# Performance work log

Measured on AMD Instinct MI355X. Metric: run time of the kernel, lower is better.

The kernel has to match this reference:

```python
import jax, jax.numpy as jnp
import numpy as np

EPS = 1e-3  # Keras BatchNormalization default epsilon


def _bn(x, gamma, beta, mean, var):
    # inference batch norm, channels-last
    inv = gamma * jax.lax.rsqrt(var + EPS)
    return x * inv + (beta - mean * inv)


def setup_inputs() -> dict:
    key = jax.random.key(0)
    ks = jax.random.split(key, 13)
    B, D, H, W, C, F = 2, 48, 48, 48, 64, 128
    return {
        "x": jax.random.normal(ks[0], (B, D, H, W, C), dtype=jnp.float32),
        "dw_kernel": jax.random.normal(ks[1], (3, 3, 3, 1, C), dtype=jnp.float32) * 0.1,
        "dw_bias": jax.random.normal(ks[2], (C,), dtype=jnp.float32) * 0.1,
        "bn1_gamma": jax.random.uniform(ks[3], (C,), dtype=jnp.float32, minval=0.5, maxval=1.5),
        "bn1_beta": jax.random.normal(ks[4], (C,), dtype=jnp.float32) * 0.1,
        "bn1_mean": jax.random.normal(ks[5], (C,), dtype=jnp.float32) * 0.1,
        "bn1_var": jax.random.uniform(ks[6], (C,), dtype=jnp.float32, minval=0.5, maxval=1.5),
        "pw_kernel": jax.random.normal(ks[7], (C, F), dtype=jnp.float32) * 0.1,
        "pw_bias": jax.random.normal(ks[8], (F,), dtype=jnp.float32) * 0.1,
        "bn2_gamma": jax.random.uniform(ks[9], (F,), dtype=jnp.float32, minval=0.5, maxval=1.5),
        "bn2_beta": jax.random.normal(ks[10], (F,), dtype=jnp.float32) * 0.1,
        "bn2_mean": jax.random.normal(ks[11], (F,), dtype=jnp.float32) * 0.1,
        "bn2_var": jax.random.uniform(ks[12], (F,), dtype=jnp.float32, minval=0.5, maxval=1.5),
    }


def reference(x, dw_kernel, dw_bias, bn1_gamma, bn1_beta, bn1_mean, bn1_var,
              pw_kernel, pw_bias, bn2_gamma, bn2_beta, bn2_mean, bn2_var):
    C = x.shape[-1]
    # True depthwise conv3d (replaces the per-channel Python loop of Conv3D(1,...))
    y = jax.lax.conv_general_dilated(
        x, dw_kernel,
        window_strides=(1, 1, 1), padding="SAME",
        dimension_numbers=("NDHWC", "DHWIO", "NDHWC"),
        feature_group_count=C,
    ) + dw_bias
    y = jax.nn.relu(_bn(y, bn1_gamma, bn1_beta, bn1_mean, bn1_var))
    # pointwise 1x1x1 conv == channel GEMM
    z = jnp.einsum("bdhwc,cf->bdhwf", y, pw_kernel) + pw_bias
    z = jax.nn.relu(_bn(z, bn2_gamma, bn2_beta, bn2_mean, bn2_var))
    return z
```

## Files before the change

### kernel.cpp

```cpp
#include <hip/hip_runtime.h>
#include <hip/hip_bf16.h>

#define EPS 1e-3f

typedef __attribute__((ext_vector_type(8))) short short8;
typedef __attribute__((ext_vector_type(4))) float v4f;

__device__ __forceinline__ unsigned short f2bf(float f) {
    unsigned int u = __float_as_uint(f);
    unsigned int r = (u + 0x7fffu + ((u >> 16) & 1u)) >> 16;
    return (unsigned short)r;
}

__global__ __launch_bounds__(256) void prep_kernel(
    const float* __restrict__ dwb,
    const float* __restrict__ g1, const float* __restrict__ b1,
    const float* __restrict__ m1, const float* __restrict__ v1,
    const float* __restrict__ pw, const float* __restrict__ pwb,
    const float* __restrict__ g2, const float* __restrict__ b2,
    const float* __restrict__ m2, const float* __restrict__ v2,
    float* __restrict__ scale1, float* __restrict__ shift1,
    float* __restrict__ s2, float* __restrict__ t2,
    unsigned short* __restrict__ Wt)
{
    int tid = threadIdx.x;
    if (blockIdx.x == 0) {
        if (tid < 64) {
            float inv = g1[tid] * rsqrtf(v1[tid] + EPS);
            scale1[tid] = inv;
            shift1[tid] = dwb[tid] * inv + b1[tid] - m1[tid] * inv;
        }
        if (tid < 128) {
            float inv = g2[tid] * rsqrtf(v2[tid] + EPS);
            s2[tid] = inv;
            t2[tid] = pwb[tid] * inv + b2[tid] - m2[tid] * inv;
        }
    }
    int idx = blockIdx.x * 256 + tid;
    int j     = idx & 7;
    int lane  = (idx >> 3) & 63;
    int kstep = (idx >> 9) & 1;
    int ntile = idx >> 10;
    int k = kstep * 32 + (lane >> 4) * 8 + j;
    int f = ntile * 16 + (lane & 15);
    Wt[idx] = f2bf(pw[k * 128 + f]);
}

__global__ __launch_bounds__(256) void fused_kernel(
    const float* __restrict__ x,
    const float* __restrict__ wgt,
    const float* __restrict__ scale1,
    const float* __restrict__ shift1,
    const unsigned short* __restrict__ Wt,
    const float* __restrict__ s2,
    const float* __restrict__ t2,
    float* __restrict__ out)
{
    __shared__ float wS[27 * 64];
    __shared__ float sS[64];
    __shared__ float tS[64];
    __shared__ unsigned short yS[64 * 72];

    int tid = threadIdx.x;
    for (int i = tid; i < 27 * 64; i += 256) wS[i] = wgt[i];
    if (tid < 64) { sS[tid] = scale1[tid]; tS[tid] = shift1[tid]; }
    __syncthreads();

    int w0 = blockIdx.x * 16;
    int h0 = blockIdx.y * 4;
    int bd = blockIdx.z;
    int b  = bd / 48;
    int d  = bd % 48;

    int tx = tid & 15;
    int ty = tid >> 4;
    int c0 = tx * 4;
    int wq = ty & 3;
    int rh = ty >> 2;
    int w0t = w0 + wq * 4;
    int h   = h0 + rh;

    float4 acc[4];
    #pragma unroll
    for (int r = 0; r < 4; ++r) acc[r] = make_float4(0.f, 0.f, 0.f, 0.f);

    float mw[6];
    int   wcl[6];
    #pragma unroll
    for (int p = 0; p < 6; ++p) {
        int zw = w0t - 1 + p;
        mw[p]  = (zw >= 0 && zw < 48) ? 1.f : 0.f;
        wcl[p] = min(max(zw, 0), 47) * 64;
    }
    float mh[3];
    int   hcl[3];
    #pragma unroll
    for (int hh = 0; hh < 3; ++hh) {
        int zh = h + hh - 1;
        mh[hh]  = (zh >= 0 && zh < 48) ? 1.f : 0.f;
        hcl[hh] = min(max(zh, 0), 47) * 48 * 64;
    }

    #pragma unroll
    for (int dd = 0; dd < 3; ++dd) {
        int zd = d + dd - 1;
        float md = (zd >= 0 && zd < 48) ? 1.f : 0.f;
        int zdc = min(max(zd, 0), 47);
        const float* dp = x + (((long)b * 48 + zdc) * 48 * 48) * 64 + c0;

        float4 xv[3][6];
        #pragma unroll
        for (int hh = 0; hh < 3; ++hh) {
            const float* rowp = dp + hcl[hh];
            #pragma unroll
            for (int p = 0; p < 6; ++p)
                xv[hh][p] = *(const float4*)(rowp + wcl[p]);
        }
        #pragma unroll
        for (int hh = 0; hh < 3; ++hh) {
            float mdh = md * mh[hh];
            #pragma unroll
            for (int p = 0; p < 6; ++p) {
                float m = mdh * mw[p];
                xv[hh][p].x *= m; xv[hh][p].y *= m;
                xv[hh][p].z *= m; xv[hh][p].w *= m;
            }
        }
        #pragma unroll
        for (int hh = 0; hh < 3; ++hh) {
            #pragma unroll
            for (int ww = 0; ww < 3; ++ww) {
                const float4 wv = *(const float4*)(&wS[((dd * 3 + hh) * 3 + ww) * 64 + c0]);
                #pragma unroll
                for (int r = 0; r < 4; ++r) {
                    acc[r].x += xv[hh][r + ww].x * wv.x;
                    acc[r].y += xv[hh][r + ww].y * wv.y;
                    acc[r].z += xv[hh][r + ww].z * wv.z;
                    acc[r].w += xv[hh][r + ww].w * wv.w;
                }
            }
        }
    }

    {
        float4 s = *(const float4*)(&sS[c0]);
        float4 t = *(const float4*)(&tS[c0]);
        #pragma unroll
        for (int r = 0; r < 4; ++r) {
            ushort4 o;
            o.x = f2bf(fmaxf(acc[r].x * s.x + t.x, 0.f));
            o.y = f2bf(fmaxf(acc[r].y * s.y + t.y, 0.f));
            o.z = f2bf(fmaxf(acc[r].z * s.z + t.z, 0.f));
            o.w = f2bf(fmaxf(acc[r].w * s.w + t.w, 0.f));
            *(ushort4*)(&yS[(ty * 4 + r) * 72 + c0]) = o;
        }
    }
    __syncthreads();

    int wv   = tid >> 6;
    int lane = tid & 63;
    int lrow = lane & 15;
    int quad = lane >> 4;

    const short8 a0 = *(const short8*)(&yS[(wv * 16 + lrow) * 72 + quad * 8]);
    const short8 a1 = *(const short8*)(&yS[(wv * 16 + lrow) * 72 + 32 + quad * 8]);

    v4f g[8];
    #pragma unroll
    for (int n = 0; n < 8; ++n) g[n] = (v4f){0.f, 0.f, 0.f, 0.f};

    #pragma unroll
    for (int n = 0; n < 8; ++n) {
        short8 b0 = *(const short8*)(Wt + ((n * 2 + 0) * 64 + lane) * 8);
        short8 b1 = *(const short8*)(Wt + ((n * 2 + 1) * 64 + lane) * 8);
        g[n] = __builtin_amdgcn_mfma_f32_16x16x32_bf16(a0, b0, g[n], 0, 0, 0);
        g[n] = __builtin_amdgcn_mfma_f32_16x16x32_bf16(a1, b1, g[n], 0, 0, 0);
    }

    long base_out = ((((long)b * 48 + d) * 48 + (h0 + wv)) * 48 + w0) * 128;
    #pragma unroll
    for (int n = 0; n < 8; ++n) {
        int f = n * 16 + lrow;
        float sf = s2[f];
        float tf = t2[f];
        #pragma unroll
        for (int r = 0; r < 4; ++r) {
            float v = fmaxf(g[n][r] * sf + tf, 0.f);
            __builtin_nontemporal_store(v, &out[base_out + (quad * 4 + r) * 128 + f]);
        }
    }
}

extern "C" void kernel_launch(void* const* d_in, const int* in_sizes, int n_in,
                              void* d_out, int out_size, void* d_ws, size_t ws_size,
                              hipStream_t stream)
{
    const float* x   = (const float*)d_in[0];
    const float* dwk = (const float*)d_in[1];
    const float* dwb = (const float*)d_in[2];
    const float* g1  = (const float*)d_in[3];
    const float* b1  = (const float*)d_in[4];
    const float* m1  = (const float*)d_in[5];
    const float* v1  = (const float*)d_in[6];
    const float* pw  = (const float*)d_in[7];
    const float* pwb = (const float*)d_in[8];
    const float* g2  = (const float*)d_in[9];
    const float* b2  = (const float*)d_in[10];
    const float* m2  = (const float*)d_in[11];
    const float* v2  = (const float*)d_in[12];

    float* outp = (float*)d_out;

    float* scale1 = (float*)d_ws;
    float* shift1 = scale1 + 64;
    float* s2     = scale1 + 128;
    float* t2     = scale1 + 256;
    unsigned short* Wt = (unsigned short*)((char*)d_ws + 2048);

    hipLaunchKernelGGL(prep_kernel, dim3(32), dim3(256), 0, stream,
                       dwb, g1, b1, m1, v1, pw, pwb, g2, b2, m2, v2,
                       scale1, shift1, s2, t2, Wt);

    hipLaunchKernelGGL(fused_kernel, dim3(3, 12, 96), dim3(256), 0, stream,
                       x, dwk, scale1, shift1, Wt, s2, t2, outp);
}
```

Measured before the change: 216.9 us.

## Remap blocks to XCDs for L2 locality, branch on boundary masks, plain stores

Flattens the grid to 1D and remaps block IDs so that each of the 8 XCDs handles a contiguous range of 12 depth slices, so neighbouring depth slices that share halo input stay in the same L2. Replaces the per-element multiplicative boundary masks with branches on depth/height validity and masks only the edge W columns, skipping FMAs for out-of-range rows. Switches the output stores from nontemporal to regular stores. These trade more branch divergence at the edges, and possible cache pollution from the output, for less redundant input traffic and arithmetic.

```diff
diff --git a/kernel.cpp b/kernel.cpp
--- a/kernel.cpp
+++ b/kernel.cpp
@@ -66,11 +66,15 @@
     if (tid < 64) { sS[tid] = scale1[tid]; tS[tid] = shift1[tid]; }
     __syncthreads();
 
-    int w0 = blockIdx.x * 16;
-    int h0 = blockIdx.y * 4;
-    int bd = blockIdx.z;
-    int b  = bd / 48;
-    int d  = bd % 48;
+    int n   = blockIdx.x;
+    int xcd = n & 7;
+    int j   = n >> 3;
+    int bd  = xcd * 12 + (j % 12);
+    int s   = j / 12;
+    int w0  = (s % 3) * 16;
+    int h0  = (s / 3) * 4;
+    int b   = bd / 48;
+    int d   = bd % 48;
 
     int tx = tid & 15;
     int ty = tid >> 4;
@@ -84,27 +88,26 @@
     #pragma unroll
     for (int r = 0; r < 4; ++r) acc[r] = make_float4(0.f, 0.f, 0.f, 0.f);
 
-    float mw[6];
-    int   wcl[6];
-    #pragma unroll
-    for (int p = 0; p < 6; ++p) {
-        int zw = w0t - 1 + p;
-        mw[p]  = (zw >= 0 && zw < 48) ? 1.f : 0.f;
-        wcl[p] = min(max(zw, 0), 47) * 64;
-    }
-    float mh[3];
-    int   hcl[3];
+    float mwL = (w0t >= 1)  ? 1.f : 0.f;
+    float mwR = (w0t <= 43) ? 1.f : 0.f;
+    int wcl[6];
+    #pragma unroll
+    for (int p = 0; p < 6; ++p)
+        wcl[p] = min(max(w0t - 1 + p, 0), 47) * 64;
+
+    bool hok[3];
+    int  hcl[3];
     #pragma unroll
     for (int hh = 0; hh < 3; ++hh) {
         int zh = h + hh - 1;
-        mh[hh]  = (zh >= 0 && zh < 48) ? 1.f : 0.f;
+        hok[hh] = (zh >= 0 && zh < 48);
         hcl[hh] = min(max(zh, 0), 47) * 48 * 64;
     }
 
     #pragma unroll
     for (int dd = 0; dd < 3; ++dd) {
         int zd = d + dd - 1;
-        float md = (zd >= 0 && zd < 48) ? 1.f : 0.f;
+        bool dok = (zd >= 0 && zd < 48);
         int zdc = min(max(zd, 0), 47);
         const float* dp = x + (((long)b * 48 + zdc) * 48 * 48) * 64 + c0;
 
@@ -116,42 +119,41 @@
             for (int p = 0; p < 6; ++p)
                 xv[hh][p] = *(const float4*)(rowp + wcl[p]);
         }
-        #pragma unroll
-        for (int hh = 0; hh < 3; ++hh) {
-            float mdh = md * mh[hh];
+
+        if (dok) {
             #pragma unroll
-            for (int p = 0; p < 6; ++p) {
-                float m = mdh * mw[p];
-                xv[hh][p].x *= m; xv[hh][p].y *= m;
-                xv[hh][p].z *= m; xv[hh][p].w *= m;
-            }
-        }
-        #pragma unroll
-        for (int hh = 0; hh < 3; ++hh) {
-            #pragma unroll
-            for (int ww = 0; ww < 3; ++ww) {
-                const float4 wv = *(const float4*)(&wS[((dd * 3 + hh) * 3 + ww) * 64 + c0]);
-                #pragma unroll
-                for (int r = 0; r < 4; ++r) {
-                    acc[r].x += xv[hh][r + ww].x * wv.x;
-                    acc[r].y += xv[hh][r + ww].y * wv.y;
-                    acc[r].z += xv[hh][r + ww].z * wv.z;
-                    acc[r].w += xv[hh][r + ww].w * wv.w;
+            for (int hh = 0; hh < 3; ++hh) {
+                if (hok[hh]) {
+                    xv[hh][0].x *= mwL; xv[hh][0].y *= mwL;
+                    xv[hh][0].z *= mwL; xv[hh][0].w *= mwL;
+                    xv[hh][5].x *= mwR; xv[hh][5].y *= mwR;
+                    xv[hh][5].z *= mwR; xv[hh][5].w *= mwR;
+                    #pragma unroll
+                    for (int ww = 0; ww < 3; ++ww) {
+                        const float4 wv = *(const float4*)(&wS[((dd * 3 + hh) * 3 + ww) * 64 + c0]);
+                        #pragma unroll
+                        for (int r = 0; r < 4; ++r) {
+                            acc[r].x += xv[hh][r + ww].x * wv.x;
+                            acc[r].y += xv[hh][r + ww].y * wv.y;
+                            acc[r].z += xv[hh][r + ww].z * wv.z;
+                            acc[r].w += xv[hh][r + ww].w * wv.w;
+                        }
+                    }
                 }
             }
         }
     }
 
     {
-        float4 s = *(const float4*)(&sS[c0]);
-        float4 t = *(const float4*)(&tS[c0]);
+        float4 s1 = *(const float4*)(&sS[c0]);
+        float4 t1 = *(const float4*)(&tS[c0]);
         #pragma unroll
         for (int r = 0; r < 4; ++r) {
             ushort4 o;
-            o.x = f2bf(fmaxf(acc[r].x * s.x + t.x, 0.f));
-            o.y = f2bf(fmaxf(acc[r].y * s.y + t.y, 0.f));
-            o.z = f2bf(fmaxf(acc[r].z * s.z + t.z, 0.f));
-            o.w = f2bf(fmaxf(acc[r].w * s.w + t.w, 0.f));
+            o.x = f2bf(fmaxf(acc[r].x * s1.x + t1.x, 0.f));
+            o.y = f2bf(fmaxf(acc[r].y * s1.y + t1.y, 0.f));
+            o.z = f2bf(fmaxf(acc[r].z * s1.z + t1.z, 0.f));
+            o.w = f2bf(fmaxf(acc[r].w * s1.w + t1.w, 0.f));
             *(ushort4*)(&yS[(ty * 4 + r) * 72 + c0]) = o;
         }
     }
@@ -167,26 +169,26 @@
 
     v4f g[8];
     #pragma unroll
-    for (int n = 0; n < 8; ++n) g[n] = (v4f){0.f, 0.f, 0.f, 0.f};
-
-    #pragma unroll
-    for (int n = 0; n < 8; ++n) {
-        short8 b0 = *(const short8*)(Wt + ((n * 2 + 0) * 64 + lane) * 8);
-        short8 b1 = *(const short8*)(Wt + ((n * 2 + 1) * 64 + lane) * 8);
-        g[n] = __builtin_amdgcn_mfma_f32_16x16x32_bf16(a0, b0, g[n], 0, 0, 0);
-        g[n] = __builtin_amdgcn_mfma_f32_16x16x32_bf16(a1, b1, g[n], 0, 0, 0);
+    for (int nn = 0; nn < 8; ++nn) g[nn] = (v4f){0.f, 0.f, 0.f, 0.f};
+
+    #pragma unroll
+    for (int nn = 0; nn < 8; ++nn) {
+        short8 b0 = *(const short8*)(Wt + ((nn * 2 + 0) * 64 + lane) * 8);
+        short8 b1 = *(const short8*)(Wt + ((nn * 2 + 1) * 64 + lane) * 8);
+        g[nn] = __builtin_amdgcn_mfma_f32_16x16x32_bf16(a0, b0, g[nn], 0, 0, 0);
+        g[nn] = __builtin_amdgcn_mfma_f32_16x16x32_bf16(a1, b1, g[nn], 0, 0, 0);
     }
 
     long base_out = ((((long)b * 48 + d) * 48 + (h0 + wv)) * 48 + w0) * 128;
     #pragma unroll
-    for (int n = 0; n < 8; ++n) {
-        int f = n * 16 + lrow;
+    for (int nn = 0; nn < 8; ++nn) {
+        int f = nn * 16 + lrow;
         float sf = s2[f];
         float tf = t2[f];
         #pragma unroll
         for (int r = 0; r < 4; ++r) {
-            float v = fmaxf(g[n][r] * sf + tf, 0.f);
-            __builtin_nontemporal_store(v, &out[base_out + (quad * 4 + r) * 128 + f]);
+            float v = fmaxf(g[nn][r] * sf + tf, 0.f);
+            out[base_out + (quad * 4 + r) * 128 + f] = v;
         }
     }
 }
@@ -221,6 +223,6 @@
                        dwb, g1, b1, m1, v1, pw, pwb, g2, b2, m2, v2,
                        scale1, shift1, s2, t2, Wt);
 
-    hipLaunchKernelGGL(fused_kernel, dim3(3, 12, 96), dim3(256), 0, stream,
+    hipLaunchKernelGGL(fused_kernel, dim3(3456), dim3(256), 0, stream,
                        x, dwk, scale1, shift1, Wt, s2, t2, outp);
 }
```

Measured after the change: 211.8 us. 2.4% less time.
